# Kernel tuning notes

Measured on AMD Instinct MI355X. Metric: run time of the kernel, lower is better.

The kernel has to match this reference:

```python
import jax, jax.numpy as jnp
import numpy as np

# Dims: N batch, C=in=out channels, T frames, V joints, S subsets, R rel_channels, H SE hidden
N, C, T, V = 256, 64, 64, 25
S, R = 3, C // 8           # num_subset, rel_channels = in_channels // rel_reduction
O = C                       # out_channels
H = max(4, O // 4)          # SE attention_channels
BN_EPS = 1e-5


def setup_inputs() -> dict:
    key = jax.random.key(0)
    ks = jax.random.split(key, 12)
    sc = 0.1
    return {
        "x":     jax.random.normal(ks[0], (N, C, T, V), jnp.float32),
        "PA":    jax.random.normal(ks[1], (S, V, V), jnp.float32) * sc,
        "alpha": jnp.ones((S,), jnp.float32),
        # per-subset stacked 1x1-conv weights (kernel_size=1 -> plain matrices)
        "w1": jax.random.normal(ks[2], (S, R, C), jnp.float32) * (2.0 / C) ** 0.5,
        "b1": jnp.zeros((S, R), jnp.float32),
        "w2": jax.random.normal(ks[3], (S, R, C), jnp.float32) * (2.0 / C) ** 0.5,
        "b2": jnp.zeros((S, R), jnp.float32),
        "w3": jax.random.normal(ks[4], (S, O, C), jnp.float32) * (2.0 / C) ** 0.5,
        "b3": jnp.zeros((S, O), jnp.float32),
        "w4": jax.random.normal(ks[5], (S, O, R), jnp.float32) * (2.0 / R) ** 0.5,
        "b4": jnp.zeros((S, O), jnp.float32),
        # final BN (eval mode: running_mean=0, running_var=1)
        "bn_w": jnp.ones((O,), jnp.float32),
        "bn_b": jnp.zeros((O,), jnp.float32),
        # SE channel attention
        "se_w1": jax.random.normal(ks[6], (H, O), jnp.float32) * (2.0 / O) ** 0.5,
        "se_b1": jnp.zeros((H,), jnp.float32),
        "se_w2": jax.random.normal(ks[7], (O, H), jnp.float32) * (2.0 / H) ** 0.5,
        "se_b2": jnp.zeros((O,), jnp.float32),
    }


def reference(x, PA, alpha, w1, b1, w2, b2, w3, b3, w4, b4,
              bn_w, bn_b, se_w1, se_b1, se_w2, se_b2):
    # --- CTRGC for all S subsets at once ---
    # conv1(x).mean(-2) == conv1 applied to x.mean over T (1x1 conv is linear)
    xm = x.mean(axis=2)                                            # [N,C,V]
    x1 = jnp.einsum('ncv,src->nsrv', xm, w1) + b1[None, :, :, None]
    x2 = jnp.einsum('ncv,src->nsrv', xm, w2) + b2[None, :, :, None]
    x3 = jnp.einsum('nctv,soc->nsotv', x, w3) + b3[None, :, :, None, None]
    # outer-difference + tanh attention map: [N,S,R,V(u),V(v)]
    att = jnp.tanh(x1[..., :, None] - x2[..., None, :])
    m = jnp.einsum('nsruv,sor->nsouv', att, w4) + b4[None, :, :, None, None]
    Asym = PA + jnp.swapaxes(PA, -1, -2)                           # A + A^T, [S,V,V]
    m = m * alpha[None, :, None, None, None] + Asym[None, :, None, :, :]
    m = jax.nn.softmax(m, axis=-2)                                 # softmax over u (dim=-2)
    # einsum 'ncuv,nctv->nctu' per subset, summed over subsets
    y = jnp.einsum('nsouv,nsotv->notu', m, x3)                     # [N,O,T,V]
    # --- BatchNorm2d (eval: mean 0, var 1) ---
    y = y / jnp.sqrt(1.0 + BN_EPS) * bn_w[None, :, None, None] + bn_b[None, :, None, None]
    # --- SE channel attention ---
    pooled = y.mean(axis=(2, 3))                                   # [N,O]
    h = jax.nn.relu(pooled @ se_w1.T + se_b1)
    se = jax.nn.sigmoid(h @ se_w2.T + se_b2)
    y = y * se[:, :, None, None]
    # --- residual (in==out -> identity down) + ReLU ---
    return jax.nn.relu(y + x)
```

## Files before the change

kernel.cpp:

```cpp
#include <hip/hip_runtime.h>

#define NN 256
#define CC 64
#define TT 64
#define VV 25
#define SS 3
#define RR 8
#define OO 64
#define HH 16

typedef _Float16 f16;
typedef _Float16 f16x8 __attribute__((ext_vector_type(8)));
typedef float f32x4 __attribute__((ext_vector_type(4)));

#define IBN 0.9999950000374997f

#define MG_NSTRIDE 153600

__device__ __forceinline__ float tanh_fast(float xx) {
  float e = __expf(2.0f * xx);
  return 1.0f - __fdividef(2.0f, e + 1.0f);
}

__global__ __launch_bounds__(256) void ka(
    const float* __restrict__ x,
    const float* __restrict__ w3, const float* __restrict__ b3,
    const float* __restrict__ bn_w, const float* __restrict__ bn_b,
    const float* __restrict__ se_w1, const float* __restrict__ se_b1,
    const float* __restrict__ se_w2, const float* __restrict__ se_b2,
    float* __restrict__ xm_g, float* __restrict__ se_g,
    f16* __restrict__ w3p_g)
{
  __shared__ float part[64][4][25];
  __shared__ float xms[1600];
  __shared__ float xmv[64], pooledv[64], hbuf[16];

  int n = blockIdx.x, tid = threadIdx.x;
  int c = tid >> 2, tq = tid & 3;

  const float* p = x + (size_t)(n*64 + c)*1600 + tq*400;
  float acc[25];
  #pragma unroll
  for (int i = 0; i < 25; ++i) acc[i] = 0.f;
  #pragma unroll
  for (int j = 0; j < 100; ++j) {
    f32x4 vv = *(const f32x4*)(p + 4*j);
    acc[(4*j + 0) % 25] += vv[0];
    acc[(4*j + 1) % 25] += vv[1];
    acc[(4*j + 2) % 25] += vv[2];
    acc[(4*j + 3) % 25] += vv[3];
  }
  #pragma unroll
  for (int i = 0; i < 25; ++i) part[c][tq][i] = acc[i];
  __syncthreads();

  for (int idx = tid; idx < 1600; idx += 256) {
    int cc = idx / 25, v = idx - cc*25;
    float s = (part[cc][0][v] + part[cc][1][v] + part[cc][2][v] + part[cc][3][v])
              * (1.0f/64.0f);
    xms[idx] = s;
    xm_g[n*1600 + idx] = s;
  }
  __syncthreads();

  if (tid < 64) {
    float s = 0.f;
    #pragma unroll
    for (int v = 0; v < 25; ++v) s += xms[tid*25 + v];
    xmv[tid] = s * (1.0f/25.0f);
  }
  __syncthreads();
  if (tid < 64) {
    int o = tid;
    float pp = b3[o] + b3[64 + o] + b3[128 + o];
    for (int cc = 0; cc < 64; ++cc)
      pp += xmv[cc] * (w3[o*64 + cc] + w3[4096 + o*64 + cc] + w3[8192 + o*64 + cc]);
    pooledv[o] = IBN * bn_w[o] * pp + bn_b[o];
  }
  __syncthreads();
  if (tid < 16) {
    float hh = se_b1[tid];
    for (int o = 0; o < 64; ++o) hh += pooledv[o] * se_w1[tid*64 + o];
    hbuf[tid] = fmaxf(hh, 0.0f);
  }
  __syncthreads();
  if (tid < 64) {
    float t = se_b2[tid];
    for (int j = 0; j < 16; ++j) t += hbuf[j] * se_w2[tid*16 + j];
    se_g[n*64 + tid] = 1.0f / (1.0f + __expf(-t));
  }

  if (n == 0) {
    for (int idx = tid; idx < 12288; idx += 256) {
      int j = idx & 7, lane = (idx >> 3) & 63, kk = (idx >> 9) & 1, mi = idx >> 10;
      int s = mi >> 2, o = ((mi & 3) << 4) + (lane & 15);
      int cc = kk*32 + ((lane >> 4) << 3) + j;
      w3p_g[idx] = (f16)w3[(s*64 + o)*64 + cc];
    }
  }
}

__global__ __launch_bounds__(256, 2) void kb(
    const float* __restrict__ xm_g, const float* __restrict__ PA,
    const float* __restrict__ alpha,
    const float* __restrict__ w1, const float* __restrict__ b1,
    const float* __restrict__ w2, const float* __restrict__ b2,
    const float* __restrict__ w4, const float* __restrict__ b4,
    f16* __restrict__ m_g)
{
  __shared__ float xms[1600];
  __shared__ float x1s[200], x2s[200];
  __shared__ float w1s[512], w2s[512];
  __shared__ float asym_s[625];
  __shared__ __attribute__((aligned(16))) float att2[5000];
  __shared__ __attribute__((aligned(16))) f16 mt[16][25][32];

  int bid = blockIdx.x;
  int n = bid & 255, s = bid >> 8;
  int tid = threadIdx.x;

  {
    const f32x4* src = (const f32x4*)(xm_g + n*1600);
    f32x4* dst = (f32x4*)xms;
    for (int i = tid; i < 400; i += 256) dst[i] = src[i];
  }
  for (int i = tid; i < 512; i += 256) {
    w1s[i] = w1[s*512 + i];
    w2s[i] = w2[s*512 + i];
  }
  for (int i = tid; i < 625; i += 256) {
    int u = i / 25, v = i - u*25;
    asym_s[i] = PA[s*625 + i] + PA[s*625 + v*25 + u];
  }
  for (int i = tid; i < 2800; i += 256) {
    int o = i / 175, rem = i - o*175, u = rem / 7, k = rem - u*7;
    mt[o][u][25 + k] = (f16)0.f;
  }
  __syncthreads();

  if (tid < 200) {
    int r = tid / 25, v = tid - r*25;
    float a1 = b1[s*8 + r], a2 = b2[s*8 + r];
    #pragma unroll
    for (int c = 0; c < 64; ++c) {
      float xv = xms[c*25 + v];
      a1 += xv * w1s[r*64 + c];
      a2 += xv * w2s[r*64 + c];
    }
    x1s[tid] = a1; x2s[tid] = a2;
  }
  __syncthreads();

  for (int idx = tid; idx < 5000; idx += 256) {
    int uv = idx >> 3, r = idx & 7;
    int u = uv / 25, v = uv - u*25;
    att2[idx] = tanh_fast(x1s[r*25 + u] - x2s[r*25 + v]);
  }
  __syncthreads();

  float alphav = alpha[s];
  f16x8* mg8 = (f16x8*)(m_g + (size_t)n*MG_NSTRIDE);

  for (int oq = 0; oq < 4; ++oq) {
    if (tid < 200) {
      int ot = tid / 25, v = tid - ot*25;
      int o0 = oq*16 + ot*2;
      float w4r[2][8], b4r[2];
      #pragma unroll
      for (int oo = 0; oo < 2; ++oo) {
        b4r[oo] = b4[s*64 + o0 + oo];
        #pragma unroll
        for (int r = 0; r < 8; ++r) w4r[oo][r] = w4[(s*64 + o0 + oo)*8 + r];
      }
      float acc[2][25];
      #pragma unroll
      for (int u = 0; u < 25; ++u) {
        const float* ap = &att2[(u*25 + v)*8];
        f32x4 a0 = *(const f32x4*)ap;
        f32x4 a1 = *(const f32x4*)(ap + 4);
        float asv = asym_s[u*25 + v];
        #pragma unroll
        for (int oo = 0; oo < 2; ++oo) {
          float t = b4r[oo];
          t += a0[0]*w4r[oo][0] + a0[1]*w4r[oo][1] + a0[2]*w4r[oo][2] + a0[3]*w4r[oo][3];
          t += a1[0]*w4r[oo][4] + a1[1]*w4r[oo][5] + a1[2]*w4r[oo][6] + a1[3]*w4r[oo][7];
          acc[oo][u] = t*alphav + asv;
        }
      }
      #pragma unroll
      for (int oo = 0; oo < 2; ++oo) {
        float mx = -1e30f;
        #pragma unroll
        for (int u = 0; u < 25; ++u) mx = fmaxf(mx, acc[oo][u]);
        float sum = 0.f;
        #pragma unroll
        for (int u = 0; u < 25; ++u) {
          float e = __expf(acc[oo][u] - mx); acc[oo][u] = e; sum += e;
        }
        float inv = 1.0f / sum;
        #pragma unroll
        for (int u = 0; u < 25; ++u) mt[ot*2 + oo][u][v] = (f16)(acc[oo][u]*inv);
      }
    }
    __syncthreads();
    for (int idx = tid; idx < 1600; idx += 256) {
      int ol = idx / 100, rem = idx - ol*100, u = rem >> 2, vc = rem & 3;
      int o = oq*16 + ol;
      mg8[((size_t)(s*64 + o)*25 + u)*4 + vc] = *(const f16x8*)&mt[ol][u][vc*8];
    }
    __syncthreads();
  }
}

struct __align__(16) SmemC {
  f16   xsT[400][72];
  f16   zs[16][16][40];
  float b3s[192];
};

__global__ __launch_bounds__(256, 2) void kc(
    const float* __restrict__ x, const float* __restrict__ b3,
    const float* __restrict__ bn_w, const float* __restrict__ bn_b,
    const f16* __restrict__ m_g, const float* __restrict__ se_g,
    const f16* __restrict__ w3p_g, float* __restrict__ out)
{
  __shared__ SmemC sm;
  int bid = blockIdx.x;
  int xcd = bid & 7, ii = bid >> 3;
  int n = xcd*32 + (ii >> 2), tt = ii & 3;
  int tid = threadIdx.x;
  int lane = tid & 63, w = tid >> 6, q = lane >> 4, l15 = lane & 15;

  {
    const float* xb = x + (size_t)n*CC*1600 + tt*400;
    #pragma unroll
    for (int it = 0; it < 50; ++it) {
      int idx = it*256 + tid;
      int cp = idx / 400, j = idx - cp*400;
      float v0 = xb[(2*cp)*1600 + j];
      float v1 = xb[(2*cp + 1)*1600 + j];
      f16* p = &sm.xsT[j][2*cp];
      p[0] = (f16)v0; p[1] = (f16)v1;
    }
    if (tid < 192) sm.b3s[tid] = b3[tid];
    for (int i = tid; i < 3840; i += 256) {
      int op = i / 240, rem = i - op*240, t = rem / 15, v = 25 + (rem - t*15);
      sm.zs[op][t][v] = (f16)0.f;
    }
  }
  __syncthreads();

  const f16x8* w3pv = (const f16x8*)w3p_g;
  const f16x8* mgv  = (const f16x8*)(m_g + (size_t)n*MG_NSTRIDE);

  for (int ob = 0; ob < 4; ++ob) {
    f32x4 yacc[4][2];
    #pragma unroll
    for (int i = 0; i < 4; ++i) {
      yacc[i][0] = (f32x4){0.f,0.f,0.f,0.f};
      yacc[i][1] = (f32x4){0.f,0.f,0.f,0.f};
    }

    for (int s = 0; s < 3; ++s) {
      f16x8 bm[4][2];
      int u2 = 16 + l15; if (u2 > 24) u2 = 24;
      #pragma unroll
      for (int i = 0; i < 4; ++i) {
        int o = ob*16 + w*4 + i;
        int rb = (s*64 + o)*25;
        bm[i][0] = mgv[(rb + l15)*4 + q];
        bm[i][1] = mgv[(rb + u2)*4 + q];
      }
      int mi = s*4 + ob;
      f16x8 a0 = w3pv[(mi*2 + 0)*64 + lane];
      f16x8 a1 = w3pv[(mi*2 + 1)*64 + lane];

      __syncthreads();

      for (int ni = w; ni < 25; ni += 4) {
        int row = ni*16 + l15;
        f16x8 bf0 = *(const f16x8*)&sm.xsT[row][q*8];
        f16x8 bf1 = *(const f16x8*)&sm.xsT[row][32 + q*8];
        f32x4 acc = (f32x4){0.f,0.f,0.f,0.f};
        acc = __builtin_amdgcn_mfma_f32_16x16x32_f16(a0, bf0, acc, 0, 0, 0);
        acc = __builtin_amdgcn_mfma_f32_16x16x32_f16(a1, bf1, acc, 0, 0, 0);
        int t = row / 25, v = row - t*25;
        #pragma unroll
        for (int rg = 0; rg < 4; ++rg) {
          int op = q*4 + rg;
          sm.zs[op][t][v] = (f16)(acc[rg] + sm.b3s[s*64 + ob*16 + op]);
        }
      }
      __syncthreads();

      #pragma unroll
      for (int i = 0; i < 4; ++i) {
        int op = w*4 + i;
        f16x8 az = *(const f16x8*)&sm.zs[op][l15][q*8];
        yacc[i][0] = __builtin_amdgcn_mfma_f32_16x16x32_f16(az, bm[i][0], yacc[i][0], 0, 0, 0);
        yacc[i][1] = __builtin_amdgcn_mfma_f32_16x16x32_f16(az, bm[i][1], yacc[i][1], 0, 0, 0);
      }
    }

    #pragma unroll
    for (int i = 0; i < 4; ++i) {
      int op = w*4 + i, o = ob*16 + op;
      float sev   = se_g[n*64 + o];
      float scale = IBN * bn_w[o] * sev;
      float bias  = bn_b[o] * sev;
      #pragma unroll
      for (int ut = 0; ut < 2; ++ut) {
        int u = ut*16 + l15;
        if (u < 25) {
          #pragma unroll
          for (int rg = 0; rg < 4; ++rg) {
            int t = q*4 + rg;
            float xres = (float)sm.xsT[t*25 + u][o];
            float val = yacc[i][ut][rg]*scale + bias + xres;
            out[(((size_t)n*64 + o)*64 + tt*16 + t)*25 + u] = fmaxf(val, 0.0f);
          }
        }
      }
    }
  }
}

extern "C" void kernel_launch(void* const* d_in, const int* in_sizes, int n_in,
                              void* d_out, int out_size, void* d_ws, size_t ws_size,
                              hipStream_t stream)
{
  const float* x    = (const float*)d_in[0];
  const float* PA   = (const float*)d_in[1];
  const float* alp  = (const float*)d_in[2];
  const float* w1   = (const float*)d_in[3];
  const float* b1   = (const float*)d_in[4];
  const float* w2   = (const float*)d_in[5];
  const float* b2   = (const float*)d_in[6];
  const float* w3   = (const float*)d_in[7];
  const float* b3   = (const float*)d_in[8];
  const float* w4   = (const float*)d_in[9];
  const float* b4   = (const float*)d_in[10];
  const float* bnw  = (const float*)d_in[11];
  const float* bnb  = (const float*)d_in[12];
  const float* sw1  = (const float*)d_in[13];
  const float* sb1  = (const float*)d_in[14];
  const float* sw2  = (const float*)d_in[15];
  const float* sb2  = (const float*)d_in[16];

  char* ws = (char*)d_ws;
  f16*   m_g   = (f16*)ws;
  float* se_g  = (float*)(ws + 78643200);
  f16*   w3p_g = (f16*)(ws + 78643200 + 65536);
  float* xm_g  = (float*)(ws + 78643200 + 65536 + 24576);

  float* out = (float*)d_out;

  ka<<<256, 256, 0, stream>>>(x, w3, b3, bnw, bnb, sw1, sb1, sw2, sb2,
                              xm_g, se_g, w3p_g);
  kb<<<768, 256, 0, stream>>>(xm_g, PA, alp, w1, b1, w2, b2, w4, b4, m_g);
  kc<<<1024, 256, 0, stream>>>(x, b3, bnw, bnb, m_g, se_g, w3p_g, out);
}
```

Baseline: 356.5 us.

## Fuse mean-pooling and attention-map kernels into a single per-batch kernel

Merges the temporal-mean/SE kernel and the per-subset attention-map kernel into one kernel with one block per batch element that loops over all three subsets. This removes a kernel launch and the global write/read of the pooled features. In exchange, the attention-map work drops from 768 blocks to 256 blocks, each doing three times the work, which reduces parallelism and latency hiding.

Measured after the change: 363.3 us. No clear change (+1.9%).

```diff
diff --git a/kernel.cpp b/kernel.cpp
--- a/kernel.cpp
+++ b/kernel.cpp
@@ -22,46 +22,79 @@
   return 1.0f - __fdividef(2.0f, e + 1.0f);
 }
 
-__global__ __launch_bounds__(256) void ka(
-    const float* __restrict__ x,
+__global__ __launch_bounds__(256) void k1(
+    const float* __restrict__ x, const float* __restrict__ PA,
+    const float* __restrict__ alpha,
+    const float* __restrict__ w1, const float* __restrict__ b1,
+    const float* __restrict__ w2, const float* __restrict__ b2,
     const float* __restrict__ w3, const float* __restrict__ b3,
+    const float* __restrict__ w4, const float* __restrict__ b4,
     const float* __restrict__ bn_w, const float* __restrict__ bn_b,
     const float* __restrict__ se_w1, const float* __restrict__ se_b1,
     const float* __restrict__ se_w2, const float* __restrict__ se_b2,
-    float* __restrict__ xm_g, float* __restrict__ se_g,
-    f16* __restrict__ w3p_g)
+    f16* __restrict__ m_g, float* __restrict__ se_g, f16* __restrict__ w3p_g)
 {
   __shared__ float part[64][4][25];
   __shared__ float xms[1600];
+  __shared__ float x1s[600], x2s[600];
+  __shared__ float w1s[1536], w2s[1536];
+  __shared__ float asym_s[1875];
+  __shared__ __attribute__((aligned(16))) float att2[5000];
+  __shared__ __attribute__((aligned(16))) f16 mt[16][25][32];
   __shared__ float xmv[64], pooledv[64], hbuf[16];
 
   int n = blockIdx.x, tid = threadIdx.x;
-  int c = tid >> 2, tq = tid & 3;
-
-  const float* p = x + (size_t)(n*64 + c)*1600 + tq*400;
-  float acc[25];
-  #pragma unroll
-  for (int i = 0; i < 25; ++i) acc[i] = 0.f;
-  #pragma unroll
-  for (int j = 0; j < 100; ++j) {
-    f32x4 vv = *(const f32x4*)(p + 4*j);
-    acc[(4*j + 0) % 25] += vv[0];
-    acc[(4*j + 1) % 25] += vv[1];
-    acc[(4*j + 2) % 25] += vv[2];
-    acc[(4*j + 3) % 25] += vv[3];
-  }
-  #pragma unroll
-  for (int i = 0; i < 25; ++i) part[c][tq][i] = acc[i];
+
+  for (int i = tid; i < 1536; i += 256) { w1s[i] = w1[i]; w2s[i] = w2[i]; }
+  for (int i = tid; i < 1875; i += 256) {
+    int s = i / 625, rem = i - s*625, u = rem / 25, v = rem - u*25;
+    asym_s[i] = PA[s*625 + u*25 + v] + PA[s*625 + v*25 + u];
+  }
+  for (int i = tid; i < 2800; i += 256) {
+    int o = i / 175, rem = i - o*175, u = rem / 7, k = rem - u*7;
+    mt[o][u][25 + k] = (f16)0.f;
+  }
+
+  {
+    int c = tid >> 2, tq = tid & 3;
+    const float* p = x + (size_t)(n*64 + c)*1600 + tq*400;
+    float acc[25];
+    #pragma unroll
+    for (int i = 0; i < 25; ++i) acc[i] = 0.f;
+    for (int blk = 0; blk < 4; ++blk) {
+      const float* pb = p + blk*100;
+      #pragma unroll
+      for (int j = 0; j < 25; ++j) {
+        f32x4 vv = *(const f32x4*)(pb + 4*j);
+        acc[(4*j + 0) % 25] += vv[0];
+        acc[(4*j + 1) % 25] += vv[1];
+        acc[(4*j + 2) % 25] += vv[2];
+        acc[(4*j + 3) % 25] += vv[3];
+      }
+    }
+    #pragma unroll
+    for (int i = 0; i < 25; ++i) part[c][tq][i] = acc[i];
+  }
   __syncthreads();
 
   for (int idx = tid; idx < 1600; idx += 256) {
     int cc = idx / 25, v = idx - cc*25;
-    float s = (part[cc][0][v] + part[cc][1][v] + part[cc][2][v] + part[cc][3][v])
-              * (1.0f/64.0f);
-    xms[idx] = s;
-    xm_g[n*1600 + idx] = s;
-  }
-  __syncthreads();
+    xms[idx] = (part[cc][0][v] + part[cc][1][v] + part[cc][2][v] + part[cc][3][v])
+               * (1.0f/64.0f);
+  }
+  __syncthreads();
+
+  for (int idx = tid; idx < 600; idx += 256) {
+    int sr = idx / 25, v = idx - sr*25;
+    float a1 = b1[sr], a2 = b2[sr];
+    #pragma unroll
+    for (int c = 0; c < 64; ++c) {
+      float xv = xms[c*25 + v];
+      a1 += xv * w1s[sr*64 + c];
+      a2 += xv * w2s[sr*64 + c];
+    }
+    x1s[idx] = a1; x2s[idx] = a2;
+  }
 
   if (tid < 64) {
     float s = 0.f;
@@ -90,6 +123,68 @@
     se_g[n*64 + tid] = 1.0f / (1.0f + __expf(-t));
   }
 
+  f16x8* mg8 = (f16x8*)(m_g + (size_t)n*MG_NSTRIDE);
+  for (int s = 0; s < 3; ++s) {
+    __syncthreads();
+    for (int idx = tid; idx < 5000; idx += 256) {
+      int uv = idx >> 3, r = idx & 7;
+      int u = uv / 25, v = uv - u*25;
+      att2[idx] = tanh_fast(x1s[(s*8 + r)*25 + u] - x2s[(s*8 + r)*25 + v]);
+    }
+    __syncthreads();
+
+    float alphav = alpha[s];
+    for (int oq = 0; oq < 4; ++oq) {
+      if (tid < 200) {
+        int ot = tid / 25, v = tid - ot*25;
+        int o0 = oq*16 + ot*2;
+        float w4r[2][8], b4r[2];
+        #pragma unroll
+        for (int oo = 0; oo < 2; ++oo) {
+          b4r[oo] = b4[s*64 + o0 + oo];
+          #pragma unroll
+          for (int r = 0; r < 8; ++r) w4r[oo][r] = w4[(s*64 + o0 + oo)*8 + r];
+        }
+        float acc[2][25];
+        #pragma unroll
+        for (int u = 0; u < 25; ++u) {
+          const float* ap = &att2[(u*25 + v)*8];
+          f32x4 a0 = *(const f32x4*)ap;
+          f32x4 a1 = *(const f32x4*)(ap + 4);
+          float asv = asym_s[s*625 + u*25 + v];
+          #pragma unroll
+          for (int oo = 0; oo < 2; ++oo) {
+            float t = b4r[oo];
+            t += a0[0]*w4r[oo][0] + a0[1]*w4r[oo][1] + a0[2]*w4r[oo][2] + a0[3]*w4r[oo][3];
+            t += a1[0]*w4r[oo][4] + a1[1]*w4r[oo][5] + a1[2]*w4r[oo][6] + a1[3]*w4r[oo][7];
+            acc[oo][u] = t*alphav + asv;
+          }
+        }
+        #pragma unroll
+        for (int oo = 0; oo < 2; ++oo) {
+          float mx = -1e30f;
+          #pragma unroll
+          for (int u = 0; u < 25; ++u) mx = fmaxf(mx, acc[oo][u]);
+          float sum = 0.f;
+          #pragma unroll
+          for (int u = 0; u < 25; ++u) {
+            float e = __expf(acc[oo][u] - mx); acc[oo][u] = e; sum += e;
+          }
+          float inv = 1.0f / sum;
+          #pragma unroll
+          for (int u = 0; u < 25; ++u) mt[ot*2 + oo][u][v] = (f16)(acc[oo][u]*inv);
+        }
+      }
+      __syncthreads();
+      for (int idx = tid; idx < 1600; idx += 256) {
+        int ol = idx / 100, rem = idx - ol*100, u = rem >> 2, vc = rem & 3;
+        int o = oq*16 + ol;
+        mg8[((size_t)(s*64 + o)*25 + u)*4 + vc] = *(const f16x8*)&mt[ol][u][vc*8];
+      }
+      __syncthreads();
+    }
+  }
+
   if (n == 0) {
     for (int idx = tid; idx < 12288; idx += 256) {
       int j = idx & 7, lane = (idx >> 3) & 63, kk = (idx >> 9) & 1, mi = idx >> 10;
@@ -97,118 +192,6 @@
       int cc = kk*32 + ((lane >> 4) << 3) + j;
       w3p_g[idx] = (f16)w3[(s*64 + o)*64 + cc];
     }
-  }
-}
-
-__global__ __launch_bounds__(256, 2) void kb(
-    const float* __restrict__ xm_g, const float* __restrict__ PA,
-    const float* __restrict__ alpha,
-    const float* __restrict__ w1, const float* __restrict__ b1,
-    const float* __restrict__ w2, const float* __restrict__ b2,
-    const float* __restrict__ w4, const float* __restrict__ b4,
-    f16* __restrict__ m_g)
-{
-  __shared__ float xms[1600];
-  __shared__ float x1s[200], x2s[200];
-  __shared__ float w1s[512], w2s[512];
-  __shared__ float asym_s[625];
-  __shared__ __attribute__((aligned(16))) float att2[5000];
-  __shared__ __attribute__((aligned(16))) f16 mt[16][25][32];
-
-  int bid = blockIdx.x;
-  int n = bid & 255, s = bid >> 8;
-  int tid = threadIdx.x;
-
-  {
-    const f32x4* src = (const f32x4*)(xm_g + n*1600);
-    f32x4* dst = (f32x4*)xms;
-    for (int i = tid; i < 400; i += 256) dst[i] = src[i];
-  }
-  for (int i = tid; i < 512; i += 256) {
-    w1s[i] = w1[s*512 + i];
-    w2s[i] = w2[s*512 + i];
-  }
-  for (int i = tid; i < 625; i += 256) {
-    int u = i / 25, v = i - u*25;
-    asym_s[i] = PA[s*625 + i] + PA[s*625 + v*25 + u];
-  }
-  for (int i = tid; i < 2800; i += 256) {
-    int o = i / 175, rem = i - o*175, u = rem / 7, k = rem - u*7;
-    mt[o][u][25 + k] = (f16)0.f;
-  }
-  __syncthreads();
-
-  if (tid < 200) {
-    int r = tid / 25, v = tid - r*25;
-    float a1 = b1[s*8 + r], a2 = b2[s*8 + r];
-    #pragma unroll
-    for (int c = 0; c < 64; ++c) {
-      float xv = xms[c*25 + v];
-      a1 += xv * w1s[r*64 + c];
-      a2 += xv * w2s[r*64 + c];
-    }
-    x1s[tid] = a1; x2s[tid] = a2;
-  }
-  __syncthreads();
-
-  for (int idx = tid; idx < 5000; idx += 256) {
-    int uv = idx >> 3, r = idx & 7;
-    int u = uv / 25, v = uv - u*25;
-    att2[idx] = tanh_fast(x1s[r*25 + u] - x2s[r*25 + v]);
-  }
-  __syncthreads();
-
-  float alphav = alpha[s];
-  f16x8* mg8 = (f16x8*)(m_g + (size_t)n*MG_NSTRIDE);
-
-  for (int oq = 0; oq < 4; ++oq) {
-    if (tid < 200) {
-      int ot = tid / 25, v = tid - ot*25;
-      int o0 = oq*16 + ot*2;
-      float w4r[2][8], b4r[2];
-      #pragma unroll
-      for (int oo = 0; oo < 2; ++oo) {
-        b4r[oo] = b4[s*64 + o0 + oo];
-        #pragma unroll
-        for (int r = 0; r < 8; ++r) w4r[oo][r] = w4[(s*64 + o0 + oo)*8 + r];
-      }
-      float acc[2][25];
-      #pragma unroll
-      for (int u = 0; u < 25; ++u) {
-        const float* ap = &att2[(u*25 + v)*8];
-        f32x4 a0 = *(const f32x4*)ap;
-        f32x4 a1 = *(const f32x4*)(ap + 4);
-        float asv = asym_s[u*25 + v];
-        #pragma unroll
-        for (int oo = 0; oo < 2; ++oo) {
-          float t = b4r[oo];
-          t += a0[0]*w4r[oo][0] + a0[1]*w4r[oo][1] + a0[2]*w4r[oo][2] + a0[3]*w4r[oo][3];
-          t += a1[0]*w4r[oo][4] + a1[1]*w4r[oo][5] + a1[2]*w4r[oo][6] + a1[3]*w4r[oo][7];
-          acc[oo][u] = t*alphav + asv;
-        }
-      }
-      #pragma unroll
-      for (int oo = 0; oo < 2; ++oo) {
-        float mx = -1e30f;
-        #pragma unroll
-        for (int u = 0; u < 25; ++u) mx = fmaxf(mx, acc[oo][u]);
-        float sum = 0.f;
-        #pragma unroll
-        for (int u = 0; u < 25; ++u) {
-          float e = __expf(acc[oo][u] - mx); acc[oo][u] = e; sum += e;
-        }
-        float inv = 1.0f / sum;
-        #pragma unroll
-        for (int u = 0; u < 25; ++u) mt[ot*2 + oo][u][v] = (f16)(acc[oo][u]*inv);
-      }
-    }
-    __syncthreads();
-    for (int idx = tid; idx < 1600; idx += 256) {
-      int ol = idx / 100, rem = idx - ol*100, u = rem >> 2, vc = rem & 3;
-      int o = oq*16 + ol;
-      mg8[((size_t)(s*64 + o)*25 + u)*4 + vc] = *(const f16x8*)&mt[ol][u][vc*8];
-    }
-    __syncthreads();
   }
 }
 
@@ -351,12 +334,10 @@
   f16*   m_g   = (f16*)ws;
   float* se_g  = (float*)(ws + 78643200);
   f16*   w3p_g = (f16*)(ws + 78643200 + 65536);
-  float* xm_g  = (float*)(ws + 78643200 + 65536 + 24576);
 
   float* out = (float*)d_out;
 
-  ka<<<256, 256, 0, stream>>>(x, w3, b3, bnw, bnb, sw1, sb1, sw2, sb2,
-                              xm_g, se_g, w3p_g);
-  kb<<<768, 256, 0, stream>>>(xm_g, PA, alp, w1, b1, w2, b2, w4, b4, m_g);
+  k1<<<256, 256, 0, stream>>>(x, PA, alp, w1, b1, w2, b2, w3, b3, w4, b4,
+                              bnw, bnb, sw1, sb1, sw2, sb2, m_g, se_g, w3p_g);
   kc<<<1024, 256, 0, stream>>>(x, b3, bnw, bnb, m_g, se_g, w3p_g, out);
 }
```
